# Kernel tuning notes

Measured on AMD Instinct MI355X. Metric: run time of the kernel, lower is better.

The kernel has to match this reference:

```python
import jax, jax.numpy as jnp
import numpy as np

E = 1024      # embed_dim
H = 16        # num_heads
D = E // H    # head_dim
F = 4096      # ff_dim
EPS = 1e-5


def setup_inputs() -> dict:
    key = jax.random.key(0)
    ks = jax.random.split(key, 12)
    s = 0.02
    return {
        "x": jax.random.normal(ks[0], (2, 2048, E), dtype=jnp.float32),
        "qkv_w": jax.random.normal(ks[1], (3 * E, E), dtype=jnp.float32) * s,
        "qkv_b": jnp.zeros((3 * E,), dtype=jnp.float32),
        "out_w": jax.random.normal(ks[2], (E, E), dtype=jnp.float32) * s,
        "out_b": jnp.zeros((E,), dtype=jnp.float32),
        "ff1_w": jax.random.normal(ks[3], (F, E), dtype=jnp.float32) * s,
        "ff1_b": jnp.zeros((F,), dtype=jnp.float32),
        "ff2_w": jax.random.normal(ks[4], (E, F), dtype=jnp.float32) * s,
        "ff2_b": jnp.zeros((E,), dtype=jnp.float32),
        "ln1_g": jnp.ones((E,), dtype=jnp.float32),
        "ln1_b": jnp.zeros((E,), dtype=jnp.float32),
        "ln2_g": jnp.ones((E,), dtype=jnp.float32),
        "ln2_b": jnp.zeros((E,), dtype=jnp.float32),
    }


def _layernorm(x, g, b):
    mu = jnp.mean(x, axis=-1, keepdims=True)
    var = jnp.mean(jnp.square(x - mu), axis=-1, keepdims=True)
    return (x - mu) * jax.lax.rsqrt(var + EPS) * g + b


def reference(x, qkv_w, qkv_b, out_w, out_b, ff1_w, ff1_b, ff2_w, ff2_b,
              ln1_g, ln1_b, ln2_g, ln2_b):
    B, S, _ = x.shape
    scale = D ** -0.5

    # --- attention sublayer (pre-LN) ---
    h = _layernorm(x, ln1_g, ln1_b)
    qkv = h @ qkv_w.T + qkv_b                          # [B,S,3E]
    qkv = qkv.reshape(B, S, 3, H, D)
    q, k, v = qkv[:, :, 0], qkv[:, :, 1], qkv[:, :, 2]  # [B,S,H,D]
    scores = jnp.einsum("bqhd,bkhd->bhqk", q, k) * scale
    attn = jax.nn.softmax(scores, axis=-1)
    o = jnp.einsum("bhqk,bkhd->bqhd", attn, v).reshape(B, S, E)
    x = x + o @ out_w.T + out_b

    # --- FFN sublayer (pre-LN, exact GELU) ---
    h = _layernorm(x, ln2_g, ln2_b)
    h = jax.nn.gelu(h @ ff1_w.T + ff1_b, approximate=False)
    x = x + h @ ff2_w.T + ff2_b
    return x
```

## Files before the change

### kernel.cpp

```cpp
#include <hip/hip_runtime.h>
#include <math.h>


typedef __attribute__((ext_vector_type(8))) short short8;
typedef __attribute__((ext_vector_type(4))) float f32x4;

__device__ __forceinline__ unsigned short f2bf(float f) {
  unsigned int u = __float_as_uint(f);
  u += 0x7fffu + ((u >> 16) & 1u);
  return (unsigned short)(u >> 16);
}

__device__ __forceinline__ short8 pack8(float4 a, float4 b) {
  short8 p;
  p[0] = (short)f2bf(a.x); p[1] = (short)f2bf(a.y);
  p[2] = (short)f2bf(a.z); p[3] = (short)f2bf(a.w);
  p[4] = (short)f2bf(b.x); p[5] = (short)f2bf(b.y);
  p[6] = (short)f2bf(b.z); p[7] = (short)f2bf(b.w);
  return p;
}

__device__ __forceinline__ float gelu_fast(float v) {
  float g = 0.7978845608f * fmaf(0.044715f * v, v * v, v);
  float den = 1.0f + exp2f(-2.885390082f * g);
  return v * __builtin_amdgcn_rcpf(den);
}

__device__ __forceinline__ void async16(const void* g, void* l) {
  __builtin_amdgcn_global_load_lds(
      (const __attribute__((address_space(1))) unsigned int*)g,
      (__attribute__((address_space(3))) unsigned int*)l, 16, 0, 0);
}

__global__ __launch_bounds__(256) void conv_all(
    const float* __restrict__ i0, unsigned short* __restrict__ o0, int n0,
    const float* __restrict__ i1, unsigned short* __restrict__ o1, int n1,
    const float* __restrict__ i2, unsigned short* __restrict__ o2, int n2,
    const float* __restrict__ i3, unsigned short* __restrict__ o3, int n3) {
  int i = blockIdx.x * 256 + threadIdx.x;
  const float* in; unsigned short* out;
  if (i < n0) { in = i0; out = o0; }
  else if ((i -= n0) < n1) { in = i1; out = o1; }
  else if ((i -= n1) < n2) { in = i2; out = o2; }
  else { i -= n2; in = i3; out = o3; if (i >= n3) return; }
  float4 v = ((const float4*)in)[i];
  ushort4 u;
  u.x = f2bf(v.x); u.y = f2bf(v.y); u.z = f2bf(v.z); u.w = f2bf(v.w);
  ((ushort4*)out)[i] = u;
}

__global__ __launch_bounds__(256) void ln_kernel(const float* __restrict__ x,
                                                 const float* __restrict__ g,
                                                 const float* __restrict__ b,
                                                 unsigned short* __restrict__ out) {
  int row = blockIdx.x;
  int t = threadIdx.x;
  const float4* x4 = (const float4*)(x + (size_t)row * 1024);
  float4 v = x4[t];
  float s1 = v.x + v.y + v.z + v.w;
  float s2 = v.x * v.x + v.y * v.y + v.z * v.z + v.w * v.w;
  for (int off = 1; off < 64; off <<= 1) {
    s1 += __shfl_xor(s1, off, 64);
    s2 += __shfl_xor(s2, off, 64);
  }
  __shared__ float r1[4], r2[4];
  int w = t >> 6, lane = t & 63;
  if (lane == 0) { r1[w] = s1; r2[w] = s2; }
  __syncthreads();
  s1 = r1[0] + r1[1] + r1[2] + r1[3];
  s2 = r2[0] + r2[1] + r2[2] + r2[3];
  float mu = s1 * (1.0f / 1024.0f);
  float var = s2 * (1.0f / 1024.0f) - mu * mu;
  float rstd = rsqrtf(var + 1e-5f);
  int c = t * 4;
  float4 gv = ((const float4*)g)[t];
  float4 bv = ((const float4*)b)[t];
  unsigned short* o = out + (size_t)row * 1024 + c;
  o[0] = f2bf((v.x - mu) * rstd * gv.x + bv.x);
  o[1] = f2bf((v.y - mu) * rstd * gv.y + bv.y);
  o[2] = f2bf((v.z - mu) * rstd * gv.z + bv.z);
  o[3] = f2bf((v.w - mu) * rstd * gv.w + bv.w);
}

template <int MODE, int BK>
__global__ __launch_bounds__(256) void gemm_bt(
    const unsigned short* __restrict__ A, const unsigned short* __restrict__ W,
    const float* __restrict__ bias, int M, int N, int K,
    const float* __restrict__ resid, float* __restrict__ out_f32,
    unsigned short* __restrict__ out_bf16,
    unsigned short* __restrict__ qbp, unsigned short* __restrict__ kbp,
    unsigned short* __restrict__ vtb) {
  constexpr int RPI = 512 / BK;
  constexpr int NI = BK / 16;
  constexpr int LPR = BK / 8;
  constexpr int KK = BK / 32;
  __shared__ __attribute__((aligned(16))) unsigned short As[2][128 * BK];
  __shared__ __attribute__((aligned(16))) unsigned short Ws[2][128 * BK];
  int tid = threadIdx.x;
  int w = tid >> 6, lane = tid & 63, quad = lane >> 4, l16 = lane & 15;
  int wrow = w >> 1, wcol = w & 1;
  int m0 = blockIdx.y * 128, n0 = blockIdx.x * 128;

  int srow = lane / LPR;
  int scol = (lane % LPR) * 8;
  const unsigned short* Ag = A + (size_t)(m0 + w * RPI + srow) * K + scol;
  const unsigned short* Wg = W + (size_t)(n0 + w * RPI + srow) * K + scol;

  f32x4 acc[4][4] = {};

  for (int i = 0; i < NI; i++) {
    async16(Ag + (size_t)(i * 4 * RPI) * K, As[0] + (i * 4 * RPI + w * RPI) * BK);
    async16(Wg + (size_t)(i * 4 * RPI) * K, Ws[0] + (i * 4 * RPI + w * RPI) * BK);
  }

  for (int k0 = 0; k0 < K; k0 += BK) {
    int buf = (k0 / BK) & 1;
    __syncthreads();
    if (k0 + BK < K) {
      int nb = buf ^ 1;
      for (int i = 0; i < NI; i++) {
        async16(Ag + (size_t)(i * 4 * RPI) * K + k0 + BK,
                As[nb] + (i * 4 * RPI + w * RPI) * BK);
        async16(Wg + (size_t)(i * 4 * RPI) * K + k0 + BK,
                Ws[nb] + (i * 4 * RPI + w * RPI) * BK);
      }
    }
    short8 af[4][KK], bf[4][KK];
    for (int i = 0; i < 4; i++)
      for (int kk = 0; kk < KK; kk++)
        af[i][kk] = *(const short8*)(As[buf] + (wrow * 64 + i * 16 + l16) * BK + kk * 32 + quad * 8);
    for (int j = 0; j < 4; j++)
      for (int kk = 0; kk < KK; kk++)
        bf[j][kk] = *(const short8*)(Ws[buf] + (wcol * 64 + j * 16 + l16) * BK + kk * 32 + quad * 8);
    for (int kk = 0; kk < KK; kk++)
      for (int i = 0; i < 4; i++)
        for (int j = 0; j < 4; j++)
          acc[i][j] = __builtin_amdgcn_mfma_f32_16x16x32_bf16(af[i][kk], bf[j][kk], acc[i][j], 0, 0, 0);
  }

  __syncthreads();
  float* ep = (w < 2) ? ((float*)As + w * 1024) : ((float*)Ws + (w - 2) * 1024);
  int orow = lane >> 2;
  int oseg = lane & 3;
  int colbase = n0 + wcol * 64;
  float bv[4];
  for (int j = 0; j < 4; j++) bv[j] = bias[colbase + j * 16 + l16];

  if (MODE == 1 || MODE == 2) {
    for (int i = 0; i < 4; i++) {
      for (int j = 0; j < 4; j++)
        for (int r = 0; r < 4; r++) {
          int row = quad * 4 + r, col = j * 16 + l16;
          float v = acc[i][j][r] + bv[j];
          if (MODE == 2) v = gelu_fast(v);
          ep[row * 64 + (((col >> 2) ^ (row & 7)) << 2) + (col & 3)] = v;
        }
      asm volatile("s_waitcnt lgkmcnt(0)" ::: "memory");
      int grow = m0 + wrow * 64 + i * 16 + orow;
      if (MODE == 1) {
        for (int t = 0; t < 4; t++) {
          int sl = t * 4 + oseg;
          float4 v = *(float4*)(ep + orow * 64 + ((sl ^ (orow & 7)) << 2));
          const float4 rv = *(const float4*)(resid + (size_t)grow * N + colbase + sl * 4);
          v.x += rv.x; v.y += rv.y; v.z += rv.z; v.w += rv.w;
          *(float4*)(out_f32 + (size_t)grow * N + colbase + sl * 4) = v;
        }
      } else {
        for (int t = 0; t < 2; t++) {
          int s0 = t * 8 + oseg * 2;
          float4 a = *(float4*)(ep + orow * 64 + ((s0 ^ (orow & 7)) << 2));
          float4 b = *(float4*)(ep + orow * 64 + (((s0 + 1) ^ (orow & 7)) << 2));
          *(short8*)(out_bf16 + (size_t)grow * N + colbase + t * 32 + oseg * 8) = pack8(a, b);
        }
      }
      asm volatile("s_waitcnt lgkmcnt(0)" ::: "memory");
    }
  } else {
    int whichW = colbase >> 10;
    int hh = (colbase & 1023) >> 6;
    int bh = (m0 >> 11) * 16 + hh;
    int sbase = (m0 & 2047) + wrow * 64;
    if (whichW < 2) {
      unsigned short* dst0 = (whichW == 0) ? qbp : kbp;
      for (int i = 0; i < 4; i++) {
        for (int j = 0; j < 4; j++)
          for (int r = 0; r < 4; r++) {
            int row = quad * 4 + r, col = j * 16 + l16;
            ep[row * 64 + (((col >> 2) ^ (row & 7)) << 2) + (col & 3)] = acc[i][j][r] + bv[j];
          }
        asm volatile("s_waitcnt lgkmcnt(0)" ::: "memory");
        int s = sbase + i * 16 + orow;
        for (int t = 0; t < 2; t++) {
          int s0 = t * 8 + oseg * 2;
          float4 a = *(float4*)(ep + orow * 64 + ((s0 ^ (orow & 7)) << 2));
          float4 b = *(float4*)(ep + orow * 64 + (((s0 + 1) ^ (orow & 7)) << 2));
          *(short8*)(dst0 + ((size_t)bh * 2048 + s) * 64 + t * 32 + oseg * 8) = pack8(a, b);
        }
        asm volatile("s_waitcnt lgkmcnt(0)" ::: "memory");
      }
    } else {
      for (int j = 0; j < 4; j++) {
        for (int i = 0; i < 4; i++) {
          float4 v4;
          v4.x = acc[i][j][0] + bv[j];
          v4.y = acc[i][j][1] + bv[j];
          v4.z = acc[i][j][2] + bv[j];
          v4.w = acc[i][j][3] + bv[j];
          *(float4*)(ep + l16 * 64 + (((i * 4 + quad) ^ (l16 & 7)) << 2)) = v4;
        }
        asm volatile("s_waitcnt lgkmcnt(0)" ::: "memory");
        int d = j * 16 + orow;
        for (int t = 0; t < 2; t++) {
          int s0 = t * 8 + oseg * 2;
          float4 a = *(float4*)(ep + orow * 64 + ((s0 ^ (orow & 7)) << 2));
          float4 b = *(float4*)(ep + orow * 64 + (((s0 + 1) ^ (orow & 7)) << 2));
          *(short8*)(vtb + ((size_t)bh * 64 + d) * 2048 + sbase + t * 32 + oseg * 8) = pack8(a, b);
        }
        asm volatile("s_waitcnt lgkmcnt(0)" ::: "memory");
      }
    }
  }
}

#define ALDP 72

__global__ __launch_bounds__(256) void attn_kernel(const unsigned short* __restrict__ qb,
                                                   const unsigned short* __restrict__ kb,
                                                   const unsigned short* __restrict__ vtb,
                                                   unsigned short* __restrict__ ob) {
  __shared__ __attribute__((aligned(16))) unsigned short Ks[2][64 * 64];
  __shared__ __attribute__((aligned(16))) unsigned short Vs[2][64 * 64];
  __shared__ __attribute__((aligned(16))) unsigned short Ps[4][2 * 16 * ALDP];

  int tid = threadIdx.x;
  int w = tid >> 6, lane = tid & 63, quad = lane >> 4, l16 = lane & 15;
  int bi = blockIdx.x;
  int bh = (bi & 7) * 4 + ((bi >> 3) & 3);
  int q0 = (bi >> 5) * 128 + w * 32;

  const unsigned short* qbase = qb + ((size_t)bh * 2048 + q0) * 64;
  const unsigned short* kbase = kb + (size_t)bh * 2048 * 64;
  const unsigned short* vbase = vtb + (size_t)bh * 64 * 2048;
  unsigned short* Pw = Ps[w];

  int srow = lane >> 3;
  int scol = ((lane & 7) ^ srow) * 8;
  const unsigned short* kg0 = kbase + (size_t)(w * 16 + srow) * 64 + scol;
  const unsigned short* kg1 = kbase + (size_t)(w * 16 + 8 + srow) * 64 + scol;
  const unsigned short* vg0 = vbase + (size_t)(w * 16 + srow) * 2048 + scol;
  const unsigned short* vg1 = vbase + (size_t)(w * 16 + 8 + srow) * 2048 + scol;

  short8 qf[2][2];
  for (int u = 0; u < 2; u++) {
    qf[u][0] = *(const short8*)(qbase + (u * 16 + l16) * 64 + quad * 8);
    qf[u][1] = *(const short8*)(qbase + (u * 16 + l16) * 64 + 32 + quad * 8);
  }

  float l0 = 0.0f, l1 = 0.0f;
  f32x4 oacc[2][4] = {};
  const float sc2 = 0.125f * 1.44269504089f;
  int sw = l16 & 7;

  async16(kg0, &Ks[0][(w * 16) * 64]);
  async16(kg1, &Ks[0][(w * 16 + 8) * 64]);
  async16(vg0, &Vs[0][(w * 16) * 64]);
  async16(vg1, &Vs[0][(w * 16 + 8) * 64]);

  for (int c0 = 0; c0 < 2048; c0 += 64) {
    int buf = (c0 >> 6) & 1;
    __syncthreads();
    if (c0 + 64 < 2048) {
      int nb = buf ^ 1;
      async16(kg0 + (size_t)(c0 + 64) * 64, &Ks[nb][(w * 16) * 64]);
      async16(kg1 + (size_t)(c0 + 64) * 64, &Ks[nb][(w * 16 + 8) * 64]);
      async16(vg0 + c0 + 64, &Vs[nb][(w * 16) * 64]);
      async16(vg1 + c0 + 64, &Vs[nb][(w * 16 + 8) * 64]);
    }
    short8 kf[4][2];
    for (int t = 0; t < 4; t++) {
      const unsigned short* kr = &Ks[buf][(t * 16 + l16) * 64];
      kf[t][0] = *(const short8*)(kr + (quad ^ sw) * 8);
      kf[t][1] = *(const short8*)(kr + ((4 + quad) ^ sw) * 8);
    }
    f32x4 s[2][4];
    for (int u = 0; u < 2; u++)
      for (int t = 0; t < 4; t++) {
        f32x4 z = {0.0f, 0.0f, 0.0f, 0.0f};
        z = __builtin_amdgcn_mfma_f32_16x16x32_bf16(kf[t][0], qf[u][0], z, 0, 0, 0);
        z = __builtin_amdgcn_mfma_f32_16x16x32_bf16(kf[t][1], qf[u][1], z, 0, 0, 0);
        s[u][t] = z;
      }
    for (int u = 0; u < 2; u++) {
      float rsum = 0.0f;
      unsigned short* pr = Pw + (u * 16 + l16) * ALDP;
      for (int t = 0; t < 4; t++) {
        float p0 = exp2f(s[u][t][0] * sc2);
        float p1 = exp2f(s[u][t][1] * sc2);
        float p2 = exp2f(s[u][t][2] * sc2);
        float p3 = exp2f(s[u][t][3] * sc2);
        rsum += (p0 + p1) + (p2 + p3);
        uint2 pk;
        pk.x = __builtin_amdgcn_perm(__float_as_uint(p1), __float_as_uint(p0), 0x07060302u);
        pk.y = __builtin_amdgcn_perm(__float_as_uint(p3), __float_as_uint(p2), 0x07060302u);
        *(uint2*)(pr + t * 16 + quad * 4) = pk;
      }
      rsum += __shfl_xor(rsum, 16, 64);
      rsum += __shfl_xor(rsum, 32, 64);
      if (u == 0) l0 += rsum; else l1 += rsum;
    }
    asm volatile("s_waitcnt lgkmcnt(0)" ::: "memory");
    for (int ks = 0; ks < 2; ks++) {
      short8 af0 = *(const short8*)(Pw + l16 * ALDP + ks * 32 + quad * 8);
      short8 af1 = *(const short8*)(Pw + (16 + l16) * ALDP + ks * 32 + quad * 8);
      for (int j = 0; j < 4; j++) {
        short8 vf = *(const short8*)(&Vs[buf][(j * 16 + l16) * 64] +
                                     ((ks * 4 + quad) ^ sw) * 8);
        oacc[0][j] = __builtin_amdgcn_mfma_f32_16x16x32_bf16(af0, vf, oacc[0][j], 0, 0, 0);
        oacc[1][j] = __builtin_amdgcn_mfma_f32_16x16x32_bf16(af1, vf, oacc[1][j], 0, 0, 0);
      }
    }
  }

  float linv[2][4];
  for (int u = 0; u < 2; u++) {
    float lr = (u == 0) ? l0 : l1;
    for (int r = 0; r < 4; r++) linv[u][r] = 1.0f / __shfl(lr, quad * 4 + r, 64);
  }
  int bb = bh >> 4, hh = bh & 15;
  for (int u = 0; u < 2; u++)
    for (int j = 0; j < 4; j++)
      for (int r = 0; r < 4; r++) {
        size_t tok = (size_t)bb * 2048 + q0 + u * 16 + quad * 4 + r;
        ob[tok * 1024 + hh * 64 + j * 16 + l16] = f2bf(oacc[u][j][r] * linv[u][r]);
      }
}

extern "C" void kernel_launch(void* const* d_in, const int* in_sizes, int n_in,
                              void* d_out, int out_size, void* d_ws, size_t ws_size,
                              hipStream_t stream) {
  (void)in_sizes; (void)n_in; (void)out_size; (void)ws_size;
  const float* x     = (const float*)d_in[0];
  const float* qkv_w = (const float*)d_in[1];
  const float* qkv_b = (const float*)d_in[2];
  const float* out_w = (const float*)d_in[3];
  const float* out_b = (const float*)d_in[4];
  const float* ff1_w = (const float*)d_in[5];
  const float* ff1_b = (const float*)d_in[6];
  const float* ff2_w = (const float*)d_in[7];
  const float* ff2_b = (const float*)d_in[8];
  const float* ln1_g = (const float*)d_in[9];
  const float* ln1_b = (const float*)d_in[10];
  const float* ln2_g = (const float*)d_in[11];
  const float* ln2_b = (const float*)d_in[12];
  float* out = (float*)d_out;
  char* ws = (char*)d_ws;

  const int M = 4096;

  unsigned short* WQ = (unsigned short*)(ws + 0);
  unsigned short* WO = (unsigned short*)(ws + 6291456);
  unsigned short* W1 = (unsigned short*)(ws + 8388608);
  unsigned short* W2 = (unsigned short*)(ws + 16777216);
  unsigned short* Hb = (unsigned short*)(ws + 25165824);
  unsigned short* Qb = (unsigned short*)(ws + 33554432);
  unsigned short* Kb = (unsigned short*)(ws + 41943040);
  unsigned short* VT = (unsigned short*)(ws + 50331648);
  unsigned short* Ob = (unsigned short*)(ws + 58720256);
  float*          X1 = (float*)(ws + 67108864);
  unsigned short* Gb = (unsigned short*)(ws + 33554432);

  conv_all<<<12288, 256, 0, stream>>>(qkv_w, WQ, 786432, out_w, WO, 262144,
                                      ff1_w, W1, 1048576, ff2_w, W2, 1048576);

  ln_kernel<<<4096, 256, 0, stream>>>(x, ln1_g, ln1_b, Hb);

  gemm_bt<0, 32><<<dim3(24, 32), 256, 0, stream>>>(Hb, WQ, qkv_b, M, 3072, 1024,
                                                   nullptr, nullptr, nullptr, Qb, Kb, VT);

  attn_kernel<<<512, 256, 0, stream>>>(Qb, Kb, VT, Ob);

  gemm_bt<1, 64><<<dim3(8, 32), 256, 0, stream>>>(Ob, WO, out_b, M, 1024, 1024,
                                                  x, X1, nullptr, nullptr, nullptr, nullptr);

  ln_kernel<<<4096, 256, 0, stream>>>(X1, ln2_g, ln2_b, Hb);

  gemm_bt<2, 32><<<dim3(32, 32), 256, 0, stream>>>(Hb, W1, ff1_b, M, 4096, 1024,
                                                   nullptr, nullptr, Gb, nullptr, nullptr, nullptr);

  gemm_bt<1, 64><<<dim3(8, 32), 256, 0, stream>>>(Gb, W2, ff2_b, M, 1024, 4096,
                                                  X1, out, nullptr, nullptr, nullptr, nullptr);
}
```

Measured before the change: 390.8 us.

## Add XOR-swizzled LDS layout, BM=64 tiles and M-major block order for N=1024 GEMMs

Generalizes the GEMM over tile height BM and adds an XOR swizzle on the LDS column segments, applied both on the async global-to-LDS copy and on the fragment reads, to cut LDS bank conflicts. The two N=1024 GEMMs (out-projection and FF2) now use 64-row tiles on a 1D grid of 512 blocks instead of 256, so more blocks are available to fill the CUs. Blocks are ordered so consecutive IDs walk M with a fixed weight column tile, which is meant to improve L2 reuse of W. Smaller tiles lower per-block arithmetic intensity and add epilogue iterations.

```diff
diff --git a/kernel.cpp b/kernel.cpp
--- a/kernel.cpp
+++ b/kernel.cpp
@@ -82,7 +82,7 @@
   o[3] = f2bf((v.w - mu) * rstd * gv.w + bv.w);
 }
 
-template <int MODE, int BK>
+template <int MODE, int BM, int BK, int LIN>
 __global__ __launch_bounds__(256) void gemm_bt(
     const unsigned short* __restrict__ A, const unsigned short* __restrict__ W,
     const float* __restrict__ bias, int M, int N, int K,
@@ -90,50 +90,66 @@
     unsigned short* __restrict__ out_bf16,
     unsigned short* __restrict__ qbp, unsigned short* __restrict__ kbp,
     unsigned short* __restrict__ vtb) {
-  constexpr int RPI = 512 / BK;
-  constexpr int NI = BK / 16;
+  constexpr int MI = BM / 32;
   constexpr int LPR = BK / 8;
+  constexpr int RPW = 512 / BK;
+  constexpr int RRND = 2048 / BK;
+  constexpr int NIA = BM / RRND;
+  constexpr int NIW = 128 / RRND;
   constexpr int KK = BK / 32;
-  __shared__ __attribute__((aligned(16))) unsigned short As[2][128 * BK];
+  __shared__ __attribute__((aligned(16))) unsigned short As[2][BM * BK];
   __shared__ __attribute__((aligned(16))) unsigned short Ws[2][128 * BK];
   int tid = threadIdx.x;
   int w = tid >> 6, lane = tid & 63, quad = lane >> 4, l16 = lane & 15;
   int wrow = w >> 1, wcol = w & 1;
-  int m0 = blockIdx.y * 128, n0 = blockIdx.x * 128;
+  int m0, n0;
+  if (LIN) {
+    int id = blockIdx.x;
+    int mc = M / BM;
+    m0 = (id % mc) * BM;
+    n0 = (id / mc) * 128;
+  } else {
+    m0 = blockIdx.y * BM;
+    n0 = blockIdx.x * 128;
+  }
 
   int srow = lane / LPR;
-  int scol = (lane % LPR) * 8;
-  const unsigned short* Ag = A + (size_t)(m0 + w * RPI + srow) * K + scol;
-  const unsigned short* Wg = W + (size_t)(n0 + w * RPI + srow) * K + scol;
-
-  f32x4 acc[4][4] = {};
-
-  for (int i = 0; i < NI; i++) {
-    async16(Ag + (size_t)(i * 4 * RPI) * K, As[0] + (i * 4 * RPI + w * RPI) * BK);
-    async16(Wg + (size_t)(i * 4 * RPI) * K, Ws[0] + (i * 4 * RPI + w * RPI) * BK);
-  }
+  int sseg = lane % LPR;
+  int ssw = (BK == 64) ? (srow & 7) : ((srow >> 1) & 3);
+  int scol = (sseg ^ ssw) * 8;
+  const unsigned short* Ag = A + (size_t)(m0 + w * RPW + srow) * K + scol;
+  const unsigned short* Wg = W + (size_t)(n0 + w * RPW + srow) * K + scol;
+
+  f32x4 acc[MI][4] = {};
+
+  for (int i = 0; i < NIA; i++)
+    async16(Ag + (size_t)(i * RRND) * K, As[0] + (i * RRND + w * RPW) * BK);
+  for (int i = 0; i < NIW; i++)
+    async16(Wg + (size_t)(i * RRND) * K, Ws[0] + (i * RRND + w * RPW) * BK);
+
+  int fsw = (BK == 64) ? (l16 & 7) : ((l16 >> 1) & 3);
 
   for (int k0 = 0; k0 < K; k0 += BK) {
     int buf = (k0 / BK) & 1;
     __syncthreads();
     if (k0 + BK < K) {
       int nb = buf ^ 1;
-      for (int i = 0; i < NI; i++) {
-        async16(Ag + (size_t)(i * 4 * RPI) * K + k0 + BK,
-                As[nb] + (i * 4 * RPI + w * RPI) * BK);
-        async16(Wg + (size_t)(i * 4 * RPI) * K + k0 + BK,
-                Ws[nb] + (i * 4 * RPI + w * RPI) * BK);
-      }
-    }
-    short8 af[4][KK], bf[4][KK];
-    for (int i = 0; i < 4; i++)
+      for (int i = 0; i < NIA; i++)
+        async16(Ag + (size_t)(i * RRND) * K + k0 + BK, As[nb] + (i * RRND + w * RPW) * BK);
+      for (int i = 0; i < NIW; i++)
+        async16(Wg + (size_t)(i * RRND) * K + k0 + BK, Ws[nb] + (i * RRND + w * RPW) * BK);
+    }
+    short8 af[MI][KK], bf[4][KK];
+    for (int i = 0; i < MI; i++)
       for (int kk = 0; kk < KK; kk++)
-        af[i][kk] = *(const short8*)(As[buf] + (wrow * 64 + i * 16 + l16) * BK + kk * 32 + quad * 8);
+        af[i][kk] = *(const short8*)(As[buf] + (wrow * (BM / 2) + i * 16 + l16) * BK +
+                                     ((kk * 4 + quad) ^ fsw) * 8);
     for (int j = 0; j < 4; j++)
       for (int kk = 0; kk < KK; kk++)
-        bf[j][kk] = *(const short8*)(Ws[buf] + (wcol * 64 + j * 16 + l16) * BK + kk * 32 + quad * 8);
+        bf[j][kk] = *(const short8*)(Ws[buf] + (wcol * 64 + j * 16 + l16) * BK +
+                                     ((kk * 4 + quad) ^ fsw) * 8);
     for (int kk = 0; kk < KK; kk++)
-      for (int i = 0; i < 4; i++)
+      for (int i = 0; i < MI; i++)
         for (int j = 0; j < 4; j++)
           acc[i][j] = __builtin_amdgcn_mfma_f32_16x16x32_bf16(af[i][kk], bf[j][kk], acc[i][j], 0, 0, 0);
   }
@@ -147,7 +163,7 @@
   for (int j = 0; j < 4; j++) bv[j] = bias[colbase + j * 16 + l16];
 
   if (MODE == 1 || MODE == 2) {
-    for (int i = 0; i < 4; i++) {
+    for (int i = 0; i < MI; i++) {
       for (int j = 0; j < 4; j++)
         for (int r = 0; r < 4; r++) {
           int row = quad * 4 + r, col = j * 16 + l16;
@@ -156,7 +172,7 @@
           ep[row * 64 + (((col >> 2) ^ (row & 7)) << 2) + (col & 3)] = v;
         }
       asm volatile("s_waitcnt lgkmcnt(0)" ::: "memory");
-      int grow = m0 + wrow * 64 + i * 16 + orow;
+      int grow = m0 + wrow * (BM / 2) + i * 16 + orow;
       if (MODE == 1) {
         for (int t = 0; t < 4; t++) {
           int sl = t * 4 + oseg;
@@ -179,10 +195,10 @@
     int whichW = colbase >> 10;
     int hh = (colbase & 1023) >> 6;
     int bh = (m0 >> 11) * 16 + hh;
-    int sbase = (m0 & 2047) + wrow * 64;
+    int sbase = (m0 & 2047) + wrow * (BM / 2);
     if (whichW < 2) {
       unsigned short* dst0 = (whichW == 0) ? qbp : kbp;
-      for (int i = 0; i < 4; i++) {
+      for (int i = 0; i < MI; i++) {
         for (int j = 0; j < 4; j++)
           for (int r = 0; r < 4; r++) {
             int row = quad * 4 + r, col = j * 16 + l16;
@@ -200,7 +216,7 @@
       }
     } else {
       for (int j = 0; j < 4; j++) {
-        for (int i = 0; i < 4; i++) {
+        for (int i = 0; i < MI; i++) {
           float4 v4;
           v4.x = acc[i][j][0] + bv[j];
           v4.y = acc[i][j][1] + bv[j];
@@ -374,19 +390,19 @@
 
   ln_kernel<<<4096, 256, 0, stream>>>(x, ln1_g, ln1_b, Hb);
 
-  gemm_bt<0, 32><<<dim3(24, 32), 256, 0, stream>>>(Hb, WQ, qkv_b, M, 3072, 1024,
-                                                   nullptr, nullptr, nullptr, Qb, Kb, VT);
+  gemm_bt<0, 128, 32, 0><<<dim3(24, 32), 256, 0, stream>>>(
+      Hb, WQ, qkv_b, M, 3072, 1024, nullptr, nullptr, nullptr, Qb, Kb, VT);
 
   attn_kernel<<<512, 256, 0, stream>>>(Qb, Kb, VT, Ob);
 
-  gemm_bt<1, 64><<<dim3(8, 32), 256, 0, stream>>>(Ob, WO, out_b, M, 1024, 1024,
-                                                  x, X1, nullptr, nullptr, nullptr, nullptr);
+  gemm_bt<1, 64, 64, 1><<<512, 256, 0, stream>>>(
+      Ob, WO, out_b, M, 1024, 1024, x, X1, nullptr, nullptr, nullptr, nullptr);
 
   ln_kernel<<<4096, 256, 0, stream>>>(X1, ln2_g, ln2_b, Hb);
 
-  gemm_bt<2, 32><<<dim3(32, 32), 256, 0, stream>>>(Hb, W1, ff1_b, M, 4096, 1024,
-                                                   nullptr, nullptr, Gb, nullptr, nullptr, nullptr);
-
-  gemm_bt<1, 64><<<dim3(8, 32), 256, 0, stream>>>(Gb, W2, ff2_b, M, 1024, 4096,
-                                                  X1, out, nullptr, nullptr, nullptr, nullptr);
-}
+  gemm_bt<2, 128, 32, 0><<<dim3(32, 32), 256, 0, stream>>>(
+      Hb, W1, ff1_b, M, 4096, 1024, nullptr, nullptr, Gb, nullptr, nullptr, nullptr);
+
+  gemm_bt<1, 64, 64, 1><<<512, 256, 0, stream>>>(
+      Gb, W2, ff2_b, M, 1024, 4096, X1, out, nullptr, nullptr, nullptr, nullptr);
+}
```

New measurement: 353.3 us. 1.11x faster.
